# Kernel optimization log

Measured on AMD Instinct MI355X. Metric: run time of the kernel, lower is better.

The kernel has to match this reference:

```python
import math
import jax, jax.numpy as jnp
import numpy as np

B, H, S, D = 2, 16, 2048, 64

def setup_inputs() -> dict:
    key = jax.random.key(0)
    kq, kk, kv = jax.random.split(key, 3)
    return {
        "query": jax.random.normal(kq, (B, H, S, D), dtype=jnp.float32),
        "key": jax.random.normal(kk, (B, H, S, D), dtype=jnp.float32),
        "value": jax.random.normal(kv, (B, H, S, D), dtype=jnp.float32),
        "mask": jnp.ones((B, S, 1), dtype=jnp.float32),  # padding mask, 1 = keep
        "mask_now": 0,  # 0 -> causal (tril diag=0); 1 -> strict causal (diag=-1)
    }

def reference(query, key, value, mask, mask_now):
    d_k = query.shape[-1]
    seq_len = mask.shape[1]
    # [B,H,S,S] scaled scores
    attn_scores = jnp.einsum("bhqd,bhkd->bhqk", query, key) / math.sqrt(d_k)
    diag = -1 if mask_now else 0
    triu_mask = jnp.tril(jnp.ones((seq_len, seq_len), dtype=mask.dtype), diag)  # [S,S]
    # mask[:, :, 0] -> per-query padding mask broadcast over key dim: [B,1,S,S]
    full_mask = triu_mask[None, None, :, :] * mask[:, None, :, 0:1]
    attn_scores = jnp.where(full_mask == 0, jnp.float32(-1e9), attn_scores)
    attn_scores = jax.nn.softmax(attn_scores, axis=-1)
    output = jnp.einsum("bhqk,bhkd->bhqd", attn_scores, value)
    return (output, attn_scores)
```

## Files before the change

kernel.cpp:

```cpp
#include <hip/hip_runtime.h>
#include <math.h>

#define NB 2
#define NH 16
#define SL 2048
#define DD 64
#define KC 64
#define NCH (SL / KC)
#define NT 256
#define LPS 68

typedef short bf16x8 __attribute__((ext_vector_type(8)));
typedef float f32x4  __attribute__((ext_vector_type(4)));

__device__ __forceinline__ unsigned short f2bf(float x) {
    unsigned u = __float_as_uint(x);
    u += 0x7fffu + ((u >> 16) & 1u);
    return (unsigned short)(u >> 16);
}

__global__ __launch_bounds__(256)
void cvt_bf16(const float* __restrict__ in, unsigned short* __restrict__ out,
              int n4, float scale)
{
    int i = blockIdx.x * 256 + threadIdx.x;
    if (i >= n4) return;
    float4 v = ((const float4*)in)[i];
    ushort4 o;
    o.x = f2bf(v.x * scale); o.y = f2bf(v.y * scale);
    o.z = f2bf(v.z * scale); o.w = f2bf(v.w * scale);
    ((ushort4*)out)[i] = o;
}

__global__ __launch_bounds__(256)
void transpose_v(const float* __restrict__ V, unsigned short* __restrict__ Vt)
{
    __shared__ __align__(16) unsigned short vt[64 * 72];
    const int bh = blockIdx.x >> 5;
    const int s0 = (blockIdx.x & 31) * 64;
    const int t  = threadIdx.x;

    const float4* src = (const float4*)(V + ((size_t)bh * SL + s0) * DD);
    #pragma unroll
    for (int i = 0; i < 4; ++i) {
        int idx = t + i * 256;
        int r = idx >> 4, d4 = idx & 15;
        float4 v = src[r * 16 + d4];
        vt[(d4 * 4 + 0) * 72 + r] = f2bf(v.x);
        vt[(d4 * 4 + 1) * 72 + r] = f2bf(v.y);
        vt[(d4 * 4 + 2) * 72 + r] = f2bf(v.z);
        vt[(d4 * 4 + 3) * 72 + r] = f2bf(v.w);
    }
    __syncthreads();
    const int d = t >> 2, seg = t & 3;
    unsigned short* dst = Vt + ((size_t)bh * DD + d) * SL + s0 + seg * 16;
    uint4 p0 = *(const uint4*)&vt[d * 72 + seg * 16];
    uint4 p1 = *(const uint4*)&vt[d * 72 + seg * 16 + 8];
    *(uint4*)dst = p0;
    *(uint4*)(dst + 8) = p1;
}

__global__ __launch_bounds__(NT, 4)
void attn_mfma(const unsigned short* __restrict__ Qb,
               const unsigned short* __restrict__ Kb,
               const unsigned short* __restrict__ Vt,
               const float* __restrict__ Mg,
               const int* __restrict__ MNg,
               float* __restrict__ Og)
{
    __shared__ __align__(16) float ps[4][16 * LPS];

    const int tid  = threadIdx.x;
    const int w    = tid >> 6;
    const int lane = tid & 63;
    const int l15  = lane & 15;
    const int qd   = lane >> 4;

    const int lin  = blockIdx.x;
    const int xcd  = lin & 7;
    const int iloc = lin >> 3;
    const int p    = iloc & 31;
    const int k    = iloc >> 5;
    const int bh   = xcd * 4 + k;
    const int b    = bh >> 4;
    const int role = (w + k) & 3;
    const int r0   = (role < 2) ? (p * 32 + (role & 1) * 16)
                                : (2016 - p * 32 + (role & 1) * 16);

    const int diag = (MNg[0] != 0) ? -1 : 0;

    int rlim[4]; int anyDeg = 0;
    #pragma unroll
    for (int reg = 0; reg < 4; ++reg) {
        int row = r0 + qd * 4 + reg;
        float m = Mg[(size_t)b * SL + row];
        int rl = row + diag;
        if (m == 0.0f) rl = -1;
        rlim[reg] = rl;
        anyDeg |= (rl < 0);
    }
    const bool waveDeg = __any(anyDeg);
    const int lastB = waveDeg ? (NCH - 1) : ((r0 + 15 + diag) >> 6);

    const unsigned short* Qh  = Qb + (size_t)bh * SL * DD;
    const unsigned short* Kh  = Kb + (size_t)bh * SL * DD;
    const unsigned short* Vth = Vt + (size_t)bh * DD * SL;
    float* Oo   = Og + ((size_t)bh * SL + r0) * DD;
    float* Sout = Og + (size_t)NB * NH * SL * DD
                     + (size_t)bh * SL * SL + (size_t)r0 * SL;
    float* slab = ps[w];

    const unsigned short* qrow = Qh + (size_t)(r0 + l15) * DD + qd * 8;
    bf16x8 qf0 = *(const bf16x8*)qrow;
    bf16x8 qf1 = *(const bf16x8*)(qrow + 32);

    float lacc[4] = {0.0f, 0.0f, 0.0f, 0.0f};
    const int total = (lastB + 1) * 4;

    auto ldK = [&](int it, bf16x8& f0, bf16x8& f1) {
        const unsigned short* kr = Kh + (size_t)(it * 16 + l15) * DD + qd * 8;
        f0 = *(const bf16x8*)kr;
        f1 = *(const bf16x8*)(kr + 32);
    };
    auto cmpA = [&](int it, bf16x8 f0, bf16x8 f1) {
        f32x4 acc = {0.0f, 0.0f, 0.0f, 0.0f};
        __builtin_amdgcn_s_setprio(1);
        acc = __builtin_amdgcn_mfma_f32_16x16x32_bf16(qf0, f0, acc, 0, 0, 0);
        acc = __builtin_amdgcn_mfma_f32_16x16x32_bf16(qf1, f1, acc, 0, 0, 0);
        __builtin_amdgcn_s_setprio(0);
        const int col = it * 16 + l15;
        #pragma unroll
        for (int reg = 0; reg < 4; ++reg)
            lacc[reg] += (col <= rlim[reg]) ? __builtin_exp2f(acc[reg]) : 0.0f;
    };

    {
        bf16x8 A0, A1, B0, B1;
        ldK(0, A0, A1);
        for (int it = 0; it < total; it += 2) {
            if (it + 1 < total) ldK(it + 1, B0, B1);
            cmpA(it, A0, A1);
            if (it + 2 < total) ldK(it + 2, A0, A1);
            if (it + 1 < total) cmpA(it + 1, B0, B1);
        }
    }

    float pmul[4], pfill[4];
    #pragma unroll
    for (int reg = 0; reg < 4; ++reg) {
        float s = lacc[reg];
        s += __shfl_xor(s, 1);  s += __shfl_xor(s, 2);
        s += __shfl_xor(s, 4);  s += __shfl_xor(s, 8);
        pmul[reg]  = (rlim[reg] < 0) ? 0.0f : 1.0f / s;
        pfill[reg] = (rlim[reg] < 0) ? (1.0f / (float)SL) : 0.0f;
    }

    f32x4 oacc[4];
    #pragma unroll
    for (int nt = 0; nt < 4; ++nt) oacc[nt] = (f32x4){0.0f, 0.0f, 0.0f, 0.0f};

    for (int kc = 0; kc <= lastB; ++kc) {
        const int c0 = kc * KC;
        bf16x8 kb0[2], kb1[2];
        ldK(kc * 4, kb0[0], kb1[0]);
        #pragma unroll
        for (int nt = 0; nt < 4; ++nt) {
            if (nt < 3) ldK(kc * 4 + nt + 1, kb0[(nt + 1) & 1], kb1[(nt + 1) & 1]);
            f32x4 acc = {0.0f, 0.0f, 0.0f, 0.0f};
            __builtin_amdgcn_s_setprio(1);
            acc = __builtin_amdgcn_mfma_f32_16x16x32_bf16(qf0, kb0[nt & 1], acc, 0, 0, 0);
            acc = __builtin_amdgcn_mfma_f32_16x16x32_bf16(qf1, kb1[nt & 1], acc, 0, 0, 0);
            __builtin_amdgcn_s_setprio(0);
            const int col = c0 + nt * 16 + l15;
            #pragma unroll
            for (int reg = 0; reg < 4; ++reg) {
                float val = (col <= rlim[reg]) ? __builtin_exp2f(acc[reg]) * pmul[reg]
                                               : pfill[reg];
                slab[(qd * 4 + reg) * LPS + nt * 16 + l15] = val;
            }
        }
        bf16x8 vb0[2], vb1[2];
        {
            const unsigned short* vr = Vth + (size_t)l15 * SL + c0 + qd * 8;
            vb0[0] = *(const bf16x8*)vr;
            vb1[0] = *(const bf16x8*)(vr + 32);
        }
        #pragma unroll
        for (int ii = 0; ii < 4; ++ii) {
            int idx = ii * 64 + lane;
            int rr = idx >> 4, c4 = idx & 15;
            *(float4*)(Sout + (size_t)rr * SL + c0 + c4 * 4) =
                *(const float4*)&slab[rr * LPS + c4 * 4];
        }
        bf16x8 paf[2];
        #pragma unroll
        for (int kb = 0; kb < 2; ++kb) {
            const float* pr = &slab[l15 * LPS + kb * 32 + qd * 8];
            float4 x = *(const float4*)pr;
            float4 y = *(const float4*)(pr + 4);
            bf16x8 f;
            f[0] = (short)f2bf(x.x); f[1] = (short)f2bf(x.y);
            f[2] = (short)f2bf(x.z); f[3] = (short)f2bf(x.w);
            f[4] = (short)f2bf(y.x); f[5] = (short)f2bf(y.y);
            f[6] = (short)f2bf(y.z); f[7] = (short)f2bf(y.w);
            paf[kb] = f;
        }
        #pragma unroll
        for (int nt = 0; nt < 4; ++nt) {
            if (nt < 3) {
                const unsigned short* vr = Vth + (size_t)((nt + 1) * 16 + l15) * SL + c0 + qd * 8;
                vb0[(nt + 1) & 1] = *(const bf16x8*)vr;
                vb1[(nt + 1) & 1] = *(const bf16x8*)(vr + 32);
            }
            __builtin_amdgcn_s_setprio(1);
            oacc[nt] = __builtin_amdgcn_mfma_f32_16x16x32_bf16(paf[0], vb0[nt & 1], oacc[nt], 0, 0, 0);
            oacc[nt] = __builtin_amdgcn_mfma_f32_16x16x32_bf16(paf[1], vb1[nt & 1], oacc[nt], 0, 0, 0);
            __builtin_amdgcn_s_setprio(0);
        }
    }

    {
        float4 z = make_float4(0.0f, 0.0f, 0.0f, 0.0f);
        for (int kc = lastB + 1; kc < NCH; ++kc) {
            const int c0 = kc * KC;
            #pragma unroll
            for (int ii = 0; ii < 4; ++ii) {
                int idx = ii * 64 + lane;
                int rr = idx >> 4, c4 = idx & 15;
                *(float4*)(Sout + (size_t)rr * SL + c0 + c4 * 4) = z;
            }
        }
    }

    #pragma unroll
    for (int nt = 0; nt < 4; ++nt)
        #pragma unroll
        for (int reg = 0; reg < 4; ++reg)
            slab[(qd * 4 + reg) * LPS + nt * 16 + l15] = oacc[nt][reg];
    #pragma unroll
    for (int ii = 0; ii < 4; ++ii) {
        int idx = ii * 64 + lane;
        int rr = idx >> 4, c4 = idx & 15;
        *(float4*)(Oo + (size_t)rr * DD + c4 * 4) = *(const float4*)&slab[rr * LPS + c4 * 4];
    }
}

extern "C" void kernel_launch(void* const* d_in, const int* in_sizes, int n_in,
                              void* d_out, int out_size, void* d_ws, size_t ws_size,
                              hipStream_t stream)
{
    const float* q  = (const float*)d_in[0];
    const float* k  = (const float*)d_in[1];
    const float* v  = (const float*)d_in[2];
    const float* mk = (const float*)d_in[3];
    const int*   mn = (const int*)d_in[4];
    float* out = (float*)d_out;

    const size_t nElem = (size_t)NB * NH * SL * DD;
    unsigned short* Qb = (unsigned short*)d_ws;
    unsigned short* Kp = Qb + nElem;
    unsigned short* Vp = Kp + nElem;

    const int n4 = (int)(nElem / 4);
    cvt_bf16<<<n4 / 256, 256, 0, stream>>>(q, Qb, n4, 0.125f * 1.44269504f);
    cvt_bf16<<<n4 / 256, 256, 0, stream>>>(k, Kp, n4, 1.0f);
    transpose_v<<<NB * NH * (SL / 64), 256, 0, stream>>>(v, Vp);

    attn_mfma<<<1024, NT, 0, stream>>>(Qb, Kp, Vp, mk, mn, out);
}
```

Baseline: 767.1 us.

## Split key range across wave pairs and combine partial sums via LDS

```diff
diff --git a/kernel.cpp b/kernel.cpp
--- a/kernel.cpp
+++ b/kernel.cpp
@@ -17,6 +17,10 @@
     unsigned u = __float_as_uint(x);
     u += 0x7fffu + ((u >> 16) & 1u);
     return (unsigned short)(u >> 16);
+}
+
+__device__ __forceinline__ void lds_barrier() {
+    asm volatile("s_waitcnt lgkmcnt(0)\n\ts_barrier" ::: "memory");
 }
 
 __global__ __launch_bounds__(256)
@@ -69,6 +73,7 @@
                float* __restrict__ Og)
 {
     __shared__ __align__(16) float ps[4][16 * LPS];
+    __shared__ float lsx[4][16];
 
     const int tid  = threadIdx.x;
     const int w    = tid >> 6;
@@ -79,13 +84,14 @@
     const int lin  = blockIdx.x;
     const int xcd  = lin & 7;
     const int iloc = lin >> 3;
-    const int p    = iloc & 31;
-    const int k    = iloc >> 5;
-    const int bh   = xcd * 4 + k;
+    const int bh   = xcd * 4 + (iloc >> 6);
+    const int g    = iloc & 63;
+    const int j    = (iloc >> 5) & 7;
     const int b    = bh >> 4;
-    const int role = (w + k) & 3;
-    const int r0   = (role < 2) ? (p * 32 + (role & 1) * 16)
-                                : (2016 - p * 32 + (role & 1) * 16);
+
+    const int role  = (w + j) & 3;
+    const int khalf = role & 1;
+    const int r0    = (role < 2) ? g * 16 : 2032 - g * 16;
 
     const int diag = (MNg[0] != 0) ? -1 : 0;
 
@@ -99,8 +105,12 @@
         rlim[reg] = rl;
         anyDeg |= (rl < 0);
     }
-    const bool waveDeg = __any(anyDeg);
-    const int lastB = waveDeg ? (NCH - 1) : ((r0 + 15 + diag) >> 6);
+    const bool grpDeg = __any(anyDeg);
+    const int lastB = grpDeg ? (NCH - 1) : ((r0 + 15 + diag) >> 6);
+    const int N     = lastB + 1;
+    const int kcMid = N >> 1;
+    const int kcBeg = khalf ? kcMid : 0;
+    const int kcEnd = khalf ? N : kcMid;
 
     const unsigned short* Qh  = Qb + (size_t)bh * SL * DD;
     const unsigned short* Kh  = Kb + (size_t)bh * SL * DD;
@@ -108,50 +118,64 @@
     float* Oo   = Og + ((size_t)bh * SL + r0) * DD;
     float* Sout = Og + (size_t)NB * NH * SL * DD
                      + (size_t)bh * SL * SL + (size_t)r0 * SL;
-    float* slab = ps[w];
+    float* slab = ps[role];
 
     const unsigned short* qrow = Qh + (size_t)(r0 + l15) * DD + qd * 8;
     bf16x8 qf0 = *(const bf16x8*)qrow;
     bf16x8 qf1 = *(const bf16x8*)(qrow + 32);
-
-    float lacc[4] = {0.0f, 0.0f, 0.0f, 0.0f};
-    const int total = (lastB + 1) * 4;
 
     auto ldK = [&](int it, bf16x8& f0, bf16x8& f1) {
         const unsigned short* kr = Kh + (size_t)(it * 16 + l15) * DD + qd * 8;
         f0 = *(const bf16x8*)kr;
         f1 = *(const bf16x8*)(kr + 32);
     };
-    auto cmpA = [&](int it, bf16x8 f0, bf16x8 f1) {
-        f32x4 acc = {0.0f, 0.0f, 0.0f, 0.0f};
-        __builtin_amdgcn_s_setprio(1);
-        acc = __builtin_amdgcn_mfma_f32_16x16x32_bf16(qf0, f0, acc, 0, 0, 0);
-        acc = __builtin_amdgcn_mfma_f32_16x16x32_bf16(qf1, f1, acc, 0, 0, 0);
-        __builtin_amdgcn_s_setprio(0);
-        const int col = it * 16 + l15;
-        #pragma unroll
-        for (int reg = 0; reg < 4; ++reg)
-            lacc[reg] += (col <= rlim[reg]) ? __builtin_exp2f(acc[reg]) : 0.0f;
-    };
-
+
+    float lacc[4] = {0.0f, 0.0f, 0.0f, 0.0f};
     {
-        bf16x8 A0, A1, B0, B1;
-        ldK(0, A0, A1);
-        for (int it = 0; it < total; it += 2) {
-            if (it + 1 < total) ldK(it + 1, B0, B1);
-            cmpA(it, A0, A1);
-            if (it + 2 < total) ldK(it + 2, A0, A1);
-            if (it + 1 < total) cmpA(it + 1, B0, B1);
-        }
-    }
-
-    float pmul[4], pfill[4];
+        const int t0 = kcBeg * 4;
+        const int T  = (kcEnd - kcBeg) * 4;
+        auto cmpA = [&](int it, bf16x8 f0, bf16x8 f1) {
+            f32x4 acc = {0.0f, 0.0f, 0.0f, 0.0f};
+            __builtin_amdgcn_s_setprio(1);
+            acc = __builtin_amdgcn_mfma_f32_16x16x32_bf16(qf0, f0, acc, 0, 0, 0);
+            acc = __builtin_amdgcn_mfma_f32_16x16x32_bf16(qf1, f1, acc, 0, 0, 0);
+            __builtin_amdgcn_s_setprio(0);
+            const int col = it * 16 + l15;
+            #pragma unroll
+            for (int reg = 0; reg < 4; ++reg)
+                lacc[reg] += (col <= rlim[reg]) ? __builtin_exp2f(acc[reg]) : 0.0f;
+        };
+        if (T > 0) {
+            bf16x8 A0, A1, B0, B1;
+            ldK(t0, A0, A1);
+            for (int t = 0; t < T; t += 2) {
+                if (t + 1 < T) ldK(t0 + t + 1, B0, B1);
+                cmpA(t0 + t, A0, A1);
+                if (t + 2 < T) ldK(t0 + t + 2, A0, A1);
+                if (t + 1 < T) cmpA(t0 + t + 1, B0, B1);
+            }
+        }
+    }
+
+    float lsum[4];
     #pragma unroll
     for (int reg = 0; reg < 4; ++reg) {
         float s = lacc[reg];
         s += __shfl_xor(s, 1);  s += __shfl_xor(s, 2);
         s += __shfl_xor(s, 4);  s += __shfl_xor(s, 8);
-        pmul[reg]  = (rlim[reg] < 0) ? 0.0f : 1.0f / s;
+        lsum[reg] = s;
+    }
+    if (l15 == 0) {
+        #pragma unroll
+        for (int reg = 0; reg < 4; ++reg)
+            lsx[role][qd * 4 + reg] = lsum[reg];
+    }
+    lds_barrier();
+    float pmul[4], pfill[4];
+    #pragma unroll
+    for (int reg = 0; reg < 4; ++reg) {
+        float tot = lsum[reg] + lsx[role ^ 1][qd * 4 + reg];
+        pmul[reg]  = (rlim[reg] < 0) ? 0.0f : 1.0f / tot;
         pfill[reg] = (rlim[reg] < 0) ? (1.0f / (float)SL) : 0.0f;
     }
 
@@ -159,7 +183,7 @@
     #pragma unroll
     for (int nt = 0; nt < 4; ++nt) oacc[nt] = (f32x4){0.0f, 0.0f, 0.0f, 0.0f};
 
-    for (int kc = 0; kc <= lastB; ++kc) {
+    for (int kc = kcBeg; kc < kcEnd; ++kc) {
         const int c0 = kc * KC;
         bf16x8 kb0[2], kb1[2];
         ldK(kc * 4, kb0[0], kb1[0]);
@@ -220,8 +244,11 @@
     }
 
     {
+        const int zMid = N + ((NCH - N) >> 1);
+        const int zb = khalf ? zMid : N;
+        const int ze = khalf ? NCH : zMid;
         float4 z = make_float4(0.0f, 0.0f, 0.0f, 0.0f);
-        for (int kc = lastB + 1; kc < NCH; ++kc) {
+        for (int kc = zb; kc < ze; ++kc) {
             const int c0 = kc * KC;
             #pragma unroll
             for (int ii = 0; ii < 4; ++ii) {
@@ -237,11 +264,20 @@
         #pragma unroll
         for (int reg = 0; reg < 4; ++reg)
             slab[(qd * 4 + reg) * LPS + nt * 16 + l15] = oacc[nt][reg];
-    #pragma unroll
-    for (int ii = 0; ii < 4; ++ii) {
-        int idx = ii * 64 + lane;
-        int rr = idx >> 4, c4 = idx & 15;
-        *(float4*)(Oo + (size_t)rr * DD + c4 * 4) = *(const float4*)&slab[rr * LPS + c4 * 4];
+    lds_barrier();
+    {
+        const float* sA = ps[role & ~1];
+        const float* sB = ps[role | 1];
+        #pragma unroll
+        for (int ii = 0; ii < 2; ++ii) {
+            int idx = ii * 64 + lane;
+            int rr = (idx >> 4) + khalf * 8;
+            int c4 = idx & 15;
+            float4 a = *(const float4*)&sA[rr * LPS + c4 * 4];
+            float4 bv = *(const float4*)&sB[rr * LPS + c4 * 4];
+            float4 o = make_float4(a.x + bv.x, a.y + bv.y, a.z + bv.z, a.w + bv.w);
+            *(float4*)(Oo + (size_t)rr * DD + c4 * 4) = o;
+        }
     }
 }
 
@@ -266,5 +302,5 @@
     cvt_bf16<<<n4 / 256, 256, 0, stream>>>(k, Kp, n4, 1.0f);
     transpose_v<<<NB * NH * (SL / 64), 256, 0, stream>>>(v, Vp);
 
-    attn_mfma<<<1024, NT, 0, stream>>>(Qb, Kp, Vp, mk, mn, out);
-}
+    attn_mfma<<<2048, NT, 0, stream>>>(Qb, Kp, Vp, mk, mn, out);
+}
```

New measurement: 744.5 us. 1.03x faster.
